# Kernel tuning notes

Measured on AMD Instinct MI355X. Metric: run time of the kernel, lower is better.

## Reference

```python
import jax, jax.numpy as jnp
import numpy as np

B, S, IN, H, D, STATE, PRED = 256, 512, 32, 256, 32, 4, 96


def setup_inputs() -> dict:
    key = jax.random.key(0)
    ks = jax.random.split(key, 16)
    sc = 1.0 / np.sqrt(H)

    def u(k, shape):
        return jax.random.uniform(k, shape, jnp.float32, -sc, sc)

    return {
        "x": jax.random.normal(ks[0], (B, S, IN), jnp.float32),
        # GRU layer 0
        "W_ih_l0": u(ks[1], (3 * H, IN)),
        "W_hh_l0": u(ks[2], (3 * H, H)),
        "b_ih_l0": u(ks[3], (3 * H,)),
        "b_hh_l0": u(ks[4], (3 * H,)),
        # GRU layer 1
        "W_ih_l1": u(ks[5], (3 * H, H)),
        "W_hh_l1": u(ks[6], (3 * H, H)),
        "b_ih_l1": u(ks[7], (3 * H,)),
        "b_hh_l1": u(ks[8], (3 * H,)),
        # state projection: hidden -> STATE*output_dim
        "W_proj": u(ks[9], (STATE * D, H)),
        "b_proj": u(ks[10], (STATE * D,)),
        # observation matrix, eye-initialized (output_dim, STATE)
        "C": jnp.eye(D, STATE, dtype=jnp.float32),
        "raw_level_decay": jnp.zeros((D,), jnp.float32),
        "raw_trend_decay": jnp.zeros((D,), jnp.float32),
        "raw_gamma": jnp.zeros((D,), jnp.float32),
        "omega": jnp.zeros((D,), jnp.float32),
    }


def _gru_layer(xs, W_ih, W_hh, b_ih, b_hh):
    # xs: (B, S, in_dim). Precompute input projections as one big GEMM.
    xp = jnp.einsum('bsi,gi->bsg', xs, W_ih) + b_ih  # (B, S, 3H)

    def step(h, xt):
        gh = h @ W_hh.T + b_hh  # (B, 3H)
        xr, xz, xn = jnp.split(xt, 3, axis=-1)
        hr, hz, hn = jnp.split(gh, 3, axis=-1)
        r = jax.nn.sigmoid(xr + hr)
        z = jax.nn.sigmoid(xz + hz)
        n = jnp.tanh(xn + r * hn)
        h_new = (1.0 - z) * n + z * h
        return h_new, h_new

    h0 = jnp.zeros((xs.shape[0], W_hh.shape[1]), xs.dtype)
    _, hs = jax.lax.scan(step, h0, jnp.swapaxes(xp, 0, 1))  # (S, B, H)
    return jnp.swapaxes(hs, 0, 1)  # (B, S, H)


def reference(x, W_ih_l0, W_hh_l0, b_ih_l0, b_hh_l0,
              W_ih_l1, W_hh_l1, b_ih_l1, b_hh_l1,
              W_proj, b_proj, C,
              raw_level_decay, raw_trend_decay, raw_gamma, omega):
    h1 = _gru_layer(x, W_ih_l0, W_hh_l0, b_ih_l0, b_hh_l0)
    h2 = _gru_layer(h1, W_ih_l1, W_hh_l1, b_ih_l1, b_hh_l1)
    final_h = h2[:, -1, :]  # (B, H)

    d_out = C.shape[0]
    s = (final_h @ W_proj.T + b_proj).reshape(x.shape[0], d_out, STATE)  # (B, D, 4)

    # time-invariant block-diagonal transition coefficients
    a_l = jax.nn.sigmoid(raw_level_decay) * 0.15 + 0.85
    a_t = jax.nn.sigmoid(raw_trend_decay) * 0.25 + 0.7
    g = jax.nn.sigmoid(raw_gamma) * 0.2 + 0.8
    c, sn = jnp.cos(omega), jnp.sin(omega)
    rot00, rot01 = g * c, -g * sn
    rot10, rot11 = g * sn, g * c

    def step(s, _):
        new_s = jnp.stack([
            s[..., 0] * a_l,
            s[..., 1] * a_t,
            s[..., 2] * rot00 + s[..., 3] * rot10,
            s[..., 2] * rot01 + s[..., 3] * rot11,
        ], axis=-1)
        y = jnp.einsum('ds,bds->bd', C, new_s)
        return new_s, y

    _, ys = jax.lax.scan(step, s, None, length=PRED)  # (PRED, B, D)
    return jnp.swapaxes(ys, 0, 1)  # (B, PRED, D)
```

## Files before the change

kernel.cpp:

```cpp
#include <hip/hip_runtime.h>
#include <cstdio>
#include <cstdint>

typedef _Float16 f16;
typedef f16 hf2   __attribute__((ext_vector_type(2)));
typedef f16 f16x8 __attribute__((ext_vector_type(8)));
typedef float f32x4 __attribute__((ext_vector_type(4)));
typedef unsigned int   u32;
typedef unsigned short u16;

#define B_    256
#define S_    512
#define IN_   32
#define H_    256
#define G3_   768
#define D_    32
#define PRED_ 96
#define TC_   16
#define KP_   72

#if __has_builtin(__builtin_amdgcn_fdot2)
__device__ __forceinline__ float fdot2(hf2 a, hf2 b, float c) {
  return __builtin_amdgcn_fdot2(a, b, c, false);
}
#else
__device__ __forceinline__ float fdot2(hf2 a, hf2 b, float c) {
  return c + (float)a[0] * (float)b[0] + (float)a[1] * (float)b[1];
}
#endif

__device__ __forceinline__ float sigm(float x) {
  return __builtin_amdgcn_rcpf(1.f + __expf(-x));
}
__device__ __forceinline__ float tanh_fast(float x) {
  return 1.f - 2.f * __builtin_amdgcn_rcpf(__expf(2.f * x) + 1.f);
}
__device__ __forceinline__ hf2 bc2(u32 v) { return __builtin_bit_cast(hf2, v); }

__global__ void f32_to_f16_k(const float* __restrict__ in, f16* __restrict__ out, int n) {
  int i = blockIdx.x * blockDim.x + threadIdx.x;
  if (i < n) out[i] = (f16)in[i];
}

__global__ void make_bias(const float* __restrict__ bih, const float* __restrict__ bhh,
                          float* __restrict__ out) {
  int i = blockIdx.x * blockDim.x + threadIdx.x;
  if (i < G3_) out[i] = bih[i] + (i < 512 ? bhh[i] : 0.f);
}

__device__ __forceinline__ f16x8 cvt8(const float* p) {
  float4 lo = ((const float4*)p)[0];
  float4 hi = ((const float4*)p)[1];
  f16x8 r;
  r[0] = (f16)lo.x; r[1] = (f16)lo.y; r[2] = (f16)lo.z; r[3] = (f16)lo.w;
  r[4] = (f16)hi.x; r[5] = (f16)hi.y; r[6] = (f16)hi.z; r[7] = (f16)hi.w;
  return r;
}

template <int KK>
__global__ __launch_bounds__(256) void gemm_xp(
    const void* __restrict__ Asrc, size_t aBlk, int tl_rows,
    const f16* __restrict__ Wih,
    const float* __restrict__ biasc,
    u16* __restrict__ xp) {
  const int tid = threadIdx.x;
  const int wv = tid >> 6, lane = tid & 63, lm = lane & 15, q = lane >> 4;
  const int tiles_pb = tl_rows >> 6;
  const int b = blockIdx.x / tiles_pb, hf = blockIdx.x % tiles_pb;
  const size_t arow0 = (size_t)b * aBlk + (size_t)(hf * 64) * KK;
  const size_t orow0 = (size_t)b * tl_rows + hf * 64;

#pragma unroll 1
  for (int nt = 0; nt < 12; ++nt) {
    const int n0 = wv * 192 + nt * 16;
    const f16* Bp = Wih + (size_t)(n0 + lm) * KK + q * 8;
    f32x4 acc[4];
#pragma unroll
    for (int j = 0; j < 4; ++j) acc[j] = f32x4{0.f, 0.f, 0.f, 0.f};
#pragma unroll
    for (int k0 = 0; k0 < KK; k0 += 32) {
      f16x8 bv = *(const f16x8*)(Bp + k0);
#pragma unroll
      for (int j = 0; j < 4; ++j) {
        f16x8 av;
        if constexpr (KK == 32) {
          av = cvt8((const float*)Asrc + arow0 + (size_t)(j * 16 + lm) * KK + k0 + q * 8);
        } else {
          av = *(const f16x8*)((const f16*)Asrc + arow0 + (size_t)(j * 16 + lm) * KK + k0 + q * 8);
        }
        acc[j] = __builtin_amdgcn_mfma_f32_16x16x32_f16(av, bv, acc[j], 0, 0, 0);
      }
    }
    const float bb = biasc[n0 + lm];
#pragma unroll
    for (int j = 0; j < 4; ++j)
#pragma unroll
      for (int r = 0; r < 4; ++r)
        xp[(orow0 + j * 16 + q * 4 + r) * G3_ + n0 + lm] =
            __builtin_bit_cast(u16, (f16)(acc[j][r] + bb));
  }
}

__global__ __launch_bounds__(512, 2) void gru_rec2(
    const u16* __restrict__ xp0,
    const u16* __restrict__ xp1,
    const f16* __restrict__ W0,
    const f16* __restrict__ W1,
    const float* __restrict__ bhh0,
    const float* __restrict__ bhh1,
    float* __restrict__ hst0,
    float* __restrict__ hst1,
    f16* __restrict__ h1c,
    int tl, int first0, int first1, int nwg0) {
  const int role = (int)(blockIdx.x >= (unsigned)nwg0);
  const int b = blockIdx.x - (role ? nwg0 : 0);
  const u16* xp = role ? xp1 : xp0;
  const f16* Whh16 = role ? W1 : W0;
  const float* bhh = role ? bhh1 : bhh0;
  float* hstate = role ? hst1 : hst0;
  const int first = role ? first1 : first0;

  const int tid = threadIdx.x;
  const int p2 = tid >> 2, kh = tid & 3;
  const int u0 = p2 * 2;

  uint4 w0[3][8], w1[3][8];
#pragma unroll
  for (int g = 0; g < 3; ++g)
#pragma unroll
    for (int t = 0; t < 8; ++t) {
      w0[g][t] = ((const uint4*)Whh16)[(size_t)(g * 256 + u0) * 32 + kh * 8 + t];
      w1[g][t] = ((const uint4*)Whh16)[(size_t)(g * 256 + u0 + 1) * 32 + kh * 8 + t];
    }
  const int myu = u0 + kh;
  const float bhn = (kh < 2) ? bhh[512 + myu] : 0.f;

  __shared__ u16 xbuf[TC_ * G3_];
  __shared__ __align__(16) u16 hbuf[2][4 * KP_];
  __shared__ u16 hhist[TC_ * H_];

  float h = 0.f;
  if (kh < 2) {
    h = first ? 0.f : hstate[b * H_ + myu];
    hbuf[0][(myu >> 6) * KP_ + (myu & 63)] = __builtin_bit_cast(u16, (f16)h);
  }
  int cur = 0;
  const uint4* xsrc = (const uint4*)xp + (size_t)b * tl * 96;
  const int nsub = tl / TC_;

#pragma unroll 1
  for (int c2 = 0; c2 < nsub; ++c2) {
    {
      const uint4* src = xsrc + (size_t)c2 * 1536;
      uint4* dst = (uint4*)xbuf;
      uint4 v0 = src[tid], v1 = src[512 + tid], v2 = src[1024 + tid];
      dst[tid] = v0; dst[512 + tid] = v1; dst[1024 + tid] = v2;
    }
    __syncthreads();

#pragma unroll 1
    for (int tl_i = 0; tl_i < TC_; ++tl_i) {
      const uint4* hb = (const uint4*)(hbuf[cur] + kh * KP_);
      float a0r = 0.f, a0z = 0.f, a0n = 0.f, a1r = 0.f, a1z = 0.f, a1n = 0.f;
#pragma unroll
      for (int cc = 0; cc < 8; ++cc) {
        uint4 hv = hb[cc];
        uint4 wa = w0[0][cc], wb = w0[1][cc], wc = w0[2][cc];
        uint4 wd = w1[0][cc], we = w1[1][cc], wf = w1[2][cc];
        a0r = fdot2(bc2(wa.x), bc2(hv.x), a0r);
        a0z = fdot2(bc2(wb.x), bc2(hv.x), a0z);
        a0n = fdot2(bc2(wc.x), bc2(hv.x), a0n);
        a1r = fdot2(bc2(wd.x), bc2(hv.x), a1r);
        a1z = fdot2(bc2(we.x), bc2(hv.x), a1z);
        a1n = fdot2(bc2(wf.x), bc2(hv.x), a1n);
        a0r = fdot2(bc2(wa.y), bc2(hv.y), a0r);
        a0z = fdot2(bc2(wb.y), bc2(hv.y), a0z);
        a0n = fdot2(bc2(wc.y), bc2(hv.y), a0n);
        a1r = fdot2(bc2(wd.y), bc2(hv.y), a1r);
        a1z = fdot2(bc2(we.y), bc2(hv.y), a1z);
        a1n = fdot2(bc2(wf.y), bc2(hv.y), a1n);
        a0r = fdot2(bc2(wa.z), bc2(hv.z), a0r);
        a0z = fdot2(bc2(wb.z), bc2(hv.z), a0z);
        a0n = fdot2(bc2(wc.z), bc2(hv.z), a0n);
        a1r = fdot2(bc2(wd.z), bc2(hv.z), a1r);
        a1z = fdot2(bc2(we.z), bc2(hv.z), a1z);
        a1n = fdot2(bc2(wf.z), bc2(hv.z), a1n);
        a0r = fdot2(bc2(wa.w), bc2(hv.w), a0r);
        a0z = fdot2(bc2(wb.w), bc2(hv.w), a0z);
        a0n = fdot2(bc2(wc.w), bc2(hv.w), a0n);
        a1r = fdot2(bc2(wd.w), bc2(hv.w), a1r);
        a1z = fdot2(bc2(we.w), bc2(hv.w), a1z);
        a1n = fdot2(bc2(wf.w), bc2(hv.w), a1n);
      }
      a0r += __shfl_xor(a0r, 1); a0r += __shfl_xor(a0r, 2);
      a0z += __shfl_xor(a0z, 1); a0z += __shfl_xor(a0z, 2);
      a0n += __shfl_xor(a0n, 1); a0n += __shfl_xor(a0n, 2);
      a1r += __shfl_xor(a1r, 1); a1r += __shfl_xor(a1r, 2);
      a1z += __shfl_xor(a1z, 1); a1z += __shfl_xor(a1z, 2);
      a1n += __shfl_xor(a1n, 1); a1n += __shfl_xor(a1n, 2);

      if (kh < 2) {
        const float ar = (kh == 0) ? a0r : a1r;
        const float az = (kh == 0) ? a0z : a1z;
        const float an = (kh == 0) ? a0n : a1n;
        const u16* xrow = xbuf + tl_i * G3_;
        float xr = (float)__builtin_bit_cast(f16, xrow[myu]);
        float xz = (float)__builtin_bit_cast(f16, xrow[256 + myu]);
        float xn = (float)__builtin_bit_cast(f16, xrow[512 + myu]);
        float r = sigm(xr + ar);
        float z = sigm(xz + az);
        float n = tanh_fast(xn + r * (an + bhn));
        h = n + z * (h - n);
        const u16 h16v = __builtin_bit_cast(u16, (f16)h);
        hbuf[cur ^ 1][(myu >> 6) * KP_ + (myu & 63)] = h16v;
        if (!role) hhist[tl_i * H_ + myu] = h16v;
      }
      __syncthreads();
      cur ^= 1;
    }

    if (!role) {
      uint4 hv0 = ((const uint4*)hhist)[tid];
      ((uint4*)(h1c + ((size_t)b * tl + c2 * TC_) * H_))[tid] = hv0;
    }
  }
  if (kh < 2) hstate[b * H_ + myu] = h;
}

__global__ __launch_bounds__(128) void proj_rollout(
    const float* __restrict__ hfinal, const float* __restrict__ Wp,
    const float* __restrict__ bp, const float* __restrict__ Cm,
    const float* __restrict__ rld, const float* __restrict__ rtd,
    const float* __restrict__ rg, const float* __restrict__ om,
    float* __restrict__ out) {
  const int b = blockIdx.x, tid = threadIdx.x;
  __shared__ float fh[256];
  __shared__ float sb[128];
  ((float2*)fh)[tid] = ((const float2*)(hfinal + b * 256))[tid];
  __syncthreads();
  const float4* wrow = (const float4*)(Wp + tid * 256);
  float acc = 0.f;
#pragma unroll 16
  for (int k4 = 0; k4 < 64; k4++) {
    float4 wv = wrow[k4];
    acc += wv.x * fh[4 * k4] + wv.y * fh[4 * k4 + 1] + wv.z * fh[4 * k4 + 2] +
           wv.w * fh[4 * k4 + 3];
  }
  sb[tid] = acc + bp[tid];
  __syncthreads();
  if (tid < 32) {
    const int dd = tid;
    float s0 = sb[dd * 4], s1 = sb[dd * 4 + 1], s2 = sb[dd * 4 + 2], s3 = sb[dd * 4 + 3];
    float al = sigm(rld[dd]) * 0.15f + 0.85f;
    float at = sigm(rtd[dd]) * 0.25f + 0.70f;
    float g  = sigm(rg[dd]) * 0.20f + 0.80f;
    float cw = cosf(om[dd]), sw = sinf(om[dd]);
    float r00 = g * cw, r01 = -g * sw, r10 = g * sw, r11 = g * cw;
    float c0 = Cm[dd * 4], c1 = Cm[dd * 4 + 1], c2 = Cm[dd * 4 + 2], c3 = Cm[dd * 4 + 3];
    float* op = out + (size_t)b * PRED_ * D_ + dd;
    for (int t = 0; t < PRED_; t++) {
      float n0 = s0 * al, n1 = s1 * at;
      float n2 = s2 * r00 + s3 * r10;
      float n3 = s2 * r01 + s3 * r11;
      op[(size_t)t * D_] = c0 * n0 + c1 * n1 + c2 * n2 + c3 * n3;
      s0 = n0; s1 = n1; s2 = n2; s3 = n3;
    }
  }
}

extern "C" void kernel_launch(void* const* d_in, const int* in_sizes, int n_in,
                              void* d_out, int out_size, void* d_ws,
                              size_t ws_size, hipStream_t stream) {
  (void)in_sizes; (void)n_in; (void)out_size;
  const float* x     = (const float*)d_in[0];
  const float* Wih0  = (const float*)d_in[1];
  const float* Whh0  = (const float*)d_in[2];
  const float* bih0  = (const float*)d_in[3];
  const float* bhh0  = (const float*)d_in[4];
  const float* Wih1  = (const float*)d_in[5];
  const float* Whh1  = (const float*)d_in[6];
  const float* bih1  = (const float*)d_in[7];
  const float* bhh1  = (const float*)d_in[8];
  const float* Wproj = (const float*)d_in[9];
  const float* bproj = (const float*)d_in[10];
  const float* Cm    = (const float*)d_in[11];
  const float* rld   = (const float*)d_in[12];
  const float* rtd   = (const float*)d_in[13];
  const float* rg    = (const float*)d_in[14];
  const float* om    = (const float*)d_in[15];
  float* out = (float*)d_out;

  char* ws = (char*)d_ws;
  const int TL = 64;
  const size_t wi0_off  = 0;
  const size_t wi1_off  = 49152;
  const size_t whh0_off = 442368;
  const size_t whh1_off = 835584;
  const size_t b0_off   = 1228800;
  const size_t b1_off   = 1231872;
  const size_t hs0_off  = 1234944;
  const size_t hs1_off  = 1497088;
  const size_t h1c_off  = 1759232;
  const size_t xp0_off  = 10147840;
  const size_t xp1_off  = 35313664;
  const size_t need     = 60479488;

  if (ws_size < need) {
    fprintf(stderr, "kernel_launch: ws too small: have %zu need %zu — skipping\n",
            ws_size, need);
    return;
  }

  f16* wi016   = (f16*)(ws + wi0_off);
  f16* wi116   = (f16*)(ws + wi1_off);
  f16* whh016  = (f16*)(ws + whh0_off);
  f16* whh116  = (f16*)(ws + whh1_off);
  float* bias0 = (float*)(ws + b0_off);
  float* bias1 = (float*)(ws + b1_off);
  float* hst0  = (float*)(ws + hs0_off);
  float* hst1  = (float*)(ws + hs1_off);
  f16* h1c     = (f16*)(ws + h1c_off);
  u16* xp0     = (u16*)(ws + xp0_off);
  u16* xp1     = (u16*)(ws + xp1_off);

  f32_to_f16_k<<<96, 256, 0, stream>>>(Wih0, wi016, G3_ * IN_);
  f32_to_f16_k<<<768, 256, 0, stream>>>(Wih1, wi116, G3_ * H_);
  f32_to_f16_k<<<768, 256, 0, stream>>>(Whh0, whh016, G3_ * H_);
  f32_to_f16_k<<<768, 256, 0, stream>>>(Whh1, whh116, G3_ * H_);
  make_bias<<<3, 256, 0, stream>>>(bih0, bhh0, bias0);
  make_bias<<<3, 256, 0, stream>>>(bih1, bhh1, bias1);

  const int nchunks = S_ / TL;
  gemm_xp<IN_><<<B_, 256, 0, stream>>>(
      (const void*)x, (size_t)S_ * IN_, TL, wi016, bias0, xp0);
  gru_rec2<<<B_, 512, 0, stream>>>(xp0, xp1, whh016, whh116, bhh0, bhh1,
                                   hst0, hst1, h1c, TL, 1, 0, B_);
  for (int c = 1; c < nchunks; ++c) {
    gemm_xp<H_><<<B_, 256, 0, stream>>>(
        (const void*)h1c, (size_t)TL * H_, TL, wi116, bias1, xp1);
    gemm_xp<IN_><<<B_, 256, 0, stream>>>(
        (const void*)(x + (size_t)c * TL * IN_), (size_t)S_ * IN_, TL, wi016, bias0, xp0);
    gru_rec2<<<2 * B_, 512, 0, stream>>>(xp0, xp1, whh016, whh116, bhh0, bhh1,
                                         hst0, hst1, h1c, TL, 0, (c == 1) ? 1 : 0, B_);
  }
  gemm_xp<H_><<<B_, 256, 0, stream>>>(
      (const void*)h1c, (size_t)TL * H_, TL, wi116, bias1, xp1);
  gru_rec2<<<B_, 512, 0, stream>>>(xp0, xp1, whh016, whh116, bhh0, bhh1,
                                   hst0, hst1, h1c, TL, 0, 0, 0);
  proj_rollout<<<B_, 128, 0, stream>>>(hst1, Wproj, bproj, Cm, rld, rtd, rg, om, out);
}
```

Baseline: 1.802 ms.

## Process two batch rows per GRU recurrence workgroup and use DPP reductions

```diff
diff --git a/kernel.cpp b/kernel.cpp
--- a/kernel.cpp
+++ b/kernel.cpp
@@ -28,6 +28,15 @@
   return c + (float)a[0] * (float)b[0] + (float)a[1] * (float)b[1];
 }
 #endif
+
+__device__ __forceinline__ float dpp_add_xor1(float x) {
+  int y = __builtin_amdgcn_mov_dpp(__builtin_bit_cast(int, x), 0xB1, 0xF, 0xF, true);
+  return x + __builtin_bit_cast(float, y);
+}
+__device__ __forceinline__ float dpp_add_xor2(float x) {
+  int y = __builtin_amdgcn_mov_dpp(__builtin_bit_cast(int, x), 0x4E, 0xF, 0xF, true);
+  return x + __builtin_bit_cast(float, y);
+}
 
 __device__ __forceinline__ float sigm(float x) {
   return __builtin_amdgcn_rcpf(1.f + __expf(-x));
@@ -113,7 +122,8 @@
     f16* __restrict__ h1c,
     int tl, int first0, int first1, int nwg0) {
   const int role = (int)(blockIdx.x >= (unsigned)nwg0);
-  const int b = blockIdx.x - (role ? nwg0 : 0);
+  const int wg = blockIdx.x - (role ? nwg0 : 0);
+  const int b0 = wg * 2;
   const u16* xp = role ? xp1 : xp0;
   const f16* Whh16 = role ? W1 : W0;
   const float* bhh = role ? bhh1 : bhh0;
@@ -135,24 +145,27 @@
   const int myu = u0 + kh;
   const float bhn = (kh < 2) ? bhh[512 + myu] : 0.f;
 
-  __shared__ u16 xbuf[TC_ * G3_];
-  __shared__ __align__(16) u16 hbuf[2][4 * KP_];
-  __shared__ u16 hhist[TC_ * H_];
-
-  float h = 0.f;
+  __shared__ u16 xb[2][TC_ * G3_];
+  __shared__ __align__(16) u16 hbuf[2][2][4 * KP_];
+  __shared__ u16 hhist[2][TC_ * H_];
+
+  float hA = 0.f, hB = 0.f;
   if (kh < 2) {
-    h = first ? 0.f : hstate[b * H_ + myu];
-    hbuf[0][(myu >> 6) * KP_ + (myu & 63)] = __builtin_bit_cast(u16, (f16)h);
+    hA = first ? 0.f : hstate[(b0 + 0) * H_ + myu];
+    hB = first ? 0.f : hstate[(b0 + 1) * H_ + myu];
+    const int slot = (myu >> 6) * KP_ + (myu & 63);
+    hbuf[0][0][slot] = __builtin_bit_cast(u16, (f16)hA);
+    hbuf[1][0][slot] = __builtin_bit_cast(u16, (f16)hB);
   }
   int cur = 0;
-  const uint4* xsrc = (const uint4*)xp + (size_t)b * tl * 96;
   const int nsub = tl / TC_;
 
 #pragma unroll 1
   for (int c2 = 0; c2 < nsub; ++c2) {
-    {
-      const uint4* src = xsrc + (size_t)c2 * 1536;
-      uint4* dst = (uint4*)xbuf;
+#pragma unroll
+    for (int r = 0; r < 2; ++r) {
+      const uint4* src = (const uint4*)xp + ((size_t)(b0 + r) * tl + c2 * TC_) * 96;
+      uint4* dst = (uint4*)xb[r];
       uint4 v0 = src[tid], v1 = src[512 + tid], v2 = src[1024 + tid];
       dst[tid] = v0; dst[512 + tid] = v1; dst[1024 + tid] = v2;
     }
@@ -160,71 +173,127 @@
 
 #pragma unroll 1
     for (int tl_i = 0; tl_i < TC_; ++tl_i) {
-      const uint4* hb = (const uint4*)(hbuf[cur] + kh * KP_);
+      const uint4* hbA = (const uint4*)(hbuf[0][cur] + kh * KP_);
+      const uint4* hbB = (const uint4*)(hbuf[1][cur] + kh * KP_);
       float a0r = 0.f, a0z = 0.f, a0n = 0.f, a1r = 0.f, a1z = 0.f, a1n = 0.f;
+      float b0r = 0.f, b0z = 0.f, b0n = 0.f, b1r = 0.f, b1z = 0.f, b1n = 0.f;
 #pragma unroll
       for (int cc = 0; cc < 8; ++cc) {
-        uint4 hv = hb[cc];
+        uint4 hvA = hbA[cc], hvB = hbB[cc];
         uint4 wa = w0[0][cc], wb = w0[1][cc], wc = w0[2][cc];
         uint4 wd = w1[0][cc], we = w1[1][cc], wf = w1[2][cc];
-        a0r = fdot2(bc2(wa.x), bc2(hv.x), a0r);
-        a0z = fdot2(bc2(wb.x), bc2(hv.x), a0z);
-        a0n = fdot2(bc2(wc.x), bc2(hv.x), a0n);
-        a1r = fdot2(bc2(wd.x), bc2(hv.x), a1r);
-        a1z = fdot2(bc2(we.x), bc2(hv.x), a1z);
-        a1n = fdot2(bc2(wf.x), bc2(hv.x), a1n);
-        a0r = fdot2(bc2(wa.y), bc2(hv.y), a0r);
-        a0z = fdot2(bc2(wb.y), bc2(hv.y), a0z);
-        a0n = fdot2(bc2(wc.y), bc2(hv.y), a0n);
-        a1r = fdot2(bc2(wd.y), bc2(hv.y), a1r);
-        a1z = fdot2(bc2(we.y), bc2(hv.y), a1z);
-        a1n = fdot2(bc2(wf.y), bc2(hv.y), a1n);
-        a0r = fdot2(bc2(wa.z), bc2(hv.z), a0r);
-        a0z = fdot2(bc2(wb.z), bc2(hv.z), a0z);
-        a0n = fdot2(bc2(wc.z), bc2(hv.z), a0n);
-        a1r = fdot2(bc2(wd.z), bc2(hv.z), a1r);
-        a1z = fdot2(bc2(we.z), bc2(hv.z), a1z);
-        a1n = fdot2(bc2(wf.z), bc2(hv.z), a1n);
-        a0r = fdot2(bc2(wa.w), bc2(hv.w), a0r);
-        a0z = fdot2(bc2(wb.w), bc2(hv.w), a0z);
-        a0n = fdot2(bc2(wc.w), bc2(hv.w), a0n);
-        a1r = fdot2(bc2(wd.w), bc2(hv.w), a1r);
-        a1z = fdot2(bc2(we.w), bc2(hv.w), a1z);
-        a1n = fdot2(bc2(wf.w), bc2(hv.w), a1n);
+        a0r = fdot2(bc2(wa.x), bc2(hvA.x), a0r);
+        a0z = fdot2(bc2(wb.x), bc2(hvA.x), a0z);
+        a0n = fdot2(bc2(wc.x), bc2(hvA.x), a0n);
+        a1r = fdot2(bc2(wd.x), bc2(hvA.x), a1r);
+        a1z = fdot2(bc2(we.x), bc2(hvA.x), a1z);
+        a1n = fdot2(bc2(wf.x), bc2(hvA.x), a1n);
+        a0r = fdot2(bc2(wa.y), bc2(hvA.y), a0r);
+        a0z = fdot2(bc2(wb.y), bc2(hvA.y), a0z);
+        a0n = fdot2(bc2(wc.y), bc2(hvA.y), a0n);
+        a1r = fdot2(bc2(wd.y), bc2(hvA.y), a1r);
+        a1z = fdot2(bc2(we.y), bc2(hvA.y), a1z);
+        a1n = fdot2(bc2(wf.y), bc2(hvA.y), a1n);
+        a0r = fdot2(bc2(wa.z), bc2(hvA.z), a0r);
+        a0z = fdot2(bc2(wb.z), bc2(hvA.z), a0z);
+        a0n = fdot2(bc2(wc.z), bc2(hvA.z), a0n);
+        a1r = fdot2(bc2(wd.z), bc2(hvA.z), a1r);
+        a1z = fdot2(bc2(we.z), bc2(hvA.z), a1z);
+        a1n = fdot2(bc2(wf.z), bc2(hvA.z), a1n);
+        a0r = fdot2(bc2(wa.w), bc2(hvA.w), a0r);
+        a0z = fdot2(bc2(wb.w), bc2(hvA.w), a0z);
+        a0n = fdot2(bc2(wc.w), bc2(hvA.w), a0n);
+        a1r = fdot2(bc2(wd.w), bc2(hvA.w), a1r);
+        a1z = fdot2(bc2(we.w), bc2(hvA.w), a1z);
+        a1n = fdot2(bc2(wf.w), bc2(hvA.w), a1n);
+        b0r = fdot2(bc2(wa.x), bc2(hvB.x), b0r);
+        b0z = fdot2(bc2(wb.x), bc2(hvB.x), b0z);
+        b0n = fdot2(bc2(wc.x), bc2(hvB.x), b0n);
+        b1r = fdot2(bc2(wd.x), bc2(hvB.x), b1r);
+        b1z = fdot2(bc2(we.x), bc2(hvB.x), b1z);
+        b1n = fdot2(bc2(wf.x), bc2(hvB.x), b1n);
+        b0r = fdot2(bc2(wa.y), bc2(hvB.y), b0r);
+        b0z = fdot2(bc2(wb.y), bc2(hvB.y), b0z);
+        b0n = fdot2(bc2(wc.y), bc2(hvB.y), b0n);
+        b1r = fdot2(bc2(wd.y), bc2(hvB.y), b1r);
+        b1z = fdot2(bc2(we.y), bc2(hvB.y), b1z);
+        b1n = fdot2(bc2(wf.y), bc2(hvB.y), b1n);
+        b0r = fdot2(bc2(wa.z), bc2(hvB.z), b0r);
+        b0z = fdot2(bc2(wb.z), bc2(hvB.z), b0z);
+        b0n = fdot2(bc2(wc.z), bc2(hvB.z), b0n);
+        b1r = fdot2(bc2(wd.z), bc2(hvB.z), b1r);
+        b1z = fdot2(bc2(we.z), bc2(hvB.z), b1z);
+        b1n = fdot2(bc2(wf.z), bc2(hvB.z), b1n);
+        b0r = fdot2(bc2(wa.w), bc2(hvB.w), b0r);
+        b0z = fdot2(bc2(wb.w), bc2(hvB.w), b0z);
+        b0n = fdot2(bc2(wc.w), bc2(hvB.w), b0n);
+        b1r = fdot2(bc2(wd.w), bc2(hvB.w), b1r);
+        b1z = fdot2(bc2(we.w), bc2(hvB.w), b1z);
+        b1n = fdot2(bc2(wf.w), bc2(hvB.w), b1n);
       }
-      a0r += __shfl_xor(a0r, 1); a0r += __shfl_xor(a0r, 2);
-      a0z += __shfl_xor(a0z, 1); a0z += __shfl_xor(a0z, 2);
-      a0n += __shfl_xor(a0n, 1); a0n += __shfl_xor(a0n, 2);
-      a1r += __shfl_xor(a1r, 1); a1r += __shfl_xor(a1r, 2);
-      a1z += __shfl_xor(a1z, 1); a1z += __shfl_xor(a1z, 2);
-      a1n += __shfl_xor(a1n, 1); a1n += __shfl_xor(a1n, 2);
+      a0r = dpp_add_xor2(dpp_add_xor1(a0r));
+      a0z = dpp_add_xor2(dpp_add_xor1(a0z));
+      a0n = dpp_add_xor2(dpp_add_xor1(a0n));
+      a1r = dpp_add_xor2(dpp_add_xor1(a1r));
+      a1z = dpp_add_xor2(dpp_add_xor1(a1z));
+      a1n = dpp_add_xor2(dpp_add_xor1(a1n));
+      b0r = dpp_add_xor2(dpp_add_xor1(b0r));
+      b0z = dpp_add_xor2(dpp_add_xor1(b0z));
+      b0n = dpp_add_xor2(dpp_add_xor1(b0n));
+      b1r = dpp_add_xor2(dpp_add_xor1(b1r));
+      b1z = dpp_add_xor2(dpp_add_xor1(b1z));
+      b1n = dpp_add_xor2(dpp_add_xor1(b1n));
 
       if (kh < 2) {
-        const float ar = (kh == 0) ? a0r : a1r;
-        const float az = (kh == 0) ? a0z : a1z;
-        const float an = (kh == 0) ? a0n : a1n;
-        const u16* xrow = xbuf + tl_i * G3_;
-        float xr = (float)__builtin_bit_cast(f16, xrow[myu]);
-        float xz = (float)__builtin_bit_cast(f16, xrow[256 + myu]);
-        float xn = (float)__builtin_bit_cast(f16, xrow[512 + myu]);
-        float r = sigm(xr + ar);
-        float z = sigm(xz + az);
-        float n = tanh_fast(xn + r * (an + bhn));
-        h = n + z * (h - n);
-        const u16 h16v = __builtin_bit_cast(u16, (f16)h);
-        hbuf[cur ^ 1][(myu >> 6) * KP_ + (myu & 63)] = h16v;
-        if (!role) hhist[tl_i * H_ + myu] = h16v;
+        const int slot = (myu >> 6) * KP_ + (myu & 63);
+        {
+          const float ar = (kh == 0) ? a0r : a1r;
+          const float az = (kh == 0) ? a0z : a1z;
+          const float an = (kh == 0) ? a0n : a1n;
+          const u16* xrow = xb[0] + tl_i * G3_;
+          float xr = (float)__builtin_bit_cast(f16, xrow[myu]);
+          float xz = (float)__builtin_bit_cast(f16, xrow[256 + myu]);
+          float xn = (float)__builtin_bit_cast(f16, xrow[512 + myu]);
+          float rr = sigm(xr + ar);
+          float zz = sigm(xz + az);
+          float nn = tanh_fast(xn + rr * (an + bhn));
+          hA = nn + zz * (hA - nn);
+          const u16 h16v = __builtin_bit_cast(u16, (f16)hA);
+          hbuf[0][cur ^ 1][slot] = h16v;
+          if (!role) hhist[0][tl_i * H_ + myu] = h16v;
+        }
+        {
+          const float ar = (kh == 0) ? b0r : b1r;
+          const float az = (kh == 0) ? b0z : b1z;
+          const float an = (kh == 0) ? b0n : b1n;
+          const u16* xrow = xb[1] + tl_i * G3_;
+          float xr = (float)__builtin_bit_cast(f16, xrow[myu]);
+          float xz = (float)__builtin_bit_cast(f16, xrow[256 + myu]);
+          float xn = (float)__builtin_bit_cast(f16, xrow[512 + myu]);
+          float rr = sigm(xr + ar);
+          float zz = sigm(xz + az);
+          float nn = tanh_fast(xn + rr * (an + bhn));
+          hB = nn + zz * (hB - nn);
+          const u16 h16v = __builtin_bit_cast(u16, (f16)hB);
+          hbuf[1][cur ^ 1][slot] = h16v;
+          if (!role) hhist[1][tl_i * H_ + myu] = h16v;
+        }
       }
       __syncthreads();
       cur ^= 1;
     }
 
     if (!role) {
-      uint4 hv0 = ((const uint4*)hhist)[tid];
-      ((uint4*)(h1c + ((size_t)b * tl + c2 * TC_) * H_))[tid] = hv0;
-    }
-  }
-  if (kh < 2) hstate[b * H_ + myu] = h;
+      uint4 v0 = ((const uint4*)hhist)[tid];
+      uint4 v1 = ((const uint4*)hhist)[512 + tid];
+      ((uint4*)(h1c + ((size_t)(b0 + 0) * tl + c2 * TC_) * H_))[tid] = v0;
+      ((uint4*)(h1c + ((size_t)(b0 + 1) * tl + c2 * TC_) * H_))[tid] = v1;
+    }
+  }
+  if (kh < 2) {
+    hstate[(b0 + 0) * H_ + myu] = hA;
+    hstate[(b0 + 1) * H_ + myu] = hB;
+  }
 }
 
 __global__ __launch_bounds__(128) void proj_rollout(
@@ -331,21 +400,22 @@
   make_bias<<<3, 256, 0, stream>>>(bih1, bhh1, bias1);
 
   const int nchunks = S_ / TL;
+  const int NW0 = B_ / 2;
   gemm_xp<IN_><<<B_, 256, 0, stream>>>(
       (const void*)x, (size_t)S_ * IN_, TL, wi016, bias0, xp0);
-  gru_rec2<<<B_, 512, 0, stream>>>(xp0, xp1, whh016, whh116, bhh0, bhh1,
-                                   hst0, hst1, h1c, TL, 1, 0, B_);
+  gru_rec2<<<NW0, 512, 0, stream>>>(xp0, xp1, whh016, whh116, bhh0, bhh1,
+                                    hst0, hst1, h1c, TL, 1, 0, NW0);
   for (int c = 1; c < nchunks; ++c) {
     gemm_xp<H_><<<B_, 256, 0, stream>>>(
         (const void*)h1c, (size_t)TL * H_, TL, wi116, bias1, xp1);
     gemm_xp<IN_><<<B_, 256, 0, stream>>>(
         (const void*)(x + (size_t)c * TL * IN_), (size_t)S_ * IN_, TL, wi016, bias0, xp0);
-    gru_rec2<<<2 * B_, 512, 0, stream>>>(xp0, xp1, whh016, whh116, bhh0, bhh1,
-                                         hst0, hst1, h1c, TL, 0, (c == 1) ? 1 : 0, B_);
+    gru_rec2<<<2 * NW0, 512, 0, stream>>>(xp0, xp1, whh016, whh116, bhh0, bhh1,
+                                          hst0, hst1, h1c, TL, 0, (c == 1) ? 1 : 0, NW0);
   }
   gemm_xp<H_><<<B_, 256, 0, stream>>>(
       (const void*)h1c, (size_t)TL * H_, TL, wi116, bias1, xp1);
-  gru_rec2<<<B_, 512, 0, stream>>>(xp0, xp1, whh016, whh116, bhh0, bhh1,
-                                   hst0, hst1, h1c, TL, 0, 0, 0);
+  gru_rec2<<<NW0, 512, 0, stream>>>(xp0, xp1, whh016, whh116, bhh0, bhh1,
+                                    hst0, hst1, h1c, TL, 0, 0, 0);
   proj_rollout<<<B_, 128, 0, stream>>>(hst1, Wproj, bproj, Cm, rld, rtd, rg, om, out);
 }
```

Result: faster. 1.695 ms (-5.9%).
